# Kernel optimization log

Measured on AMD Instinct MI355X. Metric: run time of the kernel, lower is better.

The kernel has to match this reference:

```python
import jax, jax.numpy as jnp
import numpy as np

TYPE_NUM = 40000
REL_NUM = 10000
N = TYPE_NUM + REL_NUM  # 50000 nodes
E = 800000              # edges (avg degree 16)
EMB, MID, OUT = 256, 256, 128


def setup_inputs() -> dict:
    key = jax.random.key(0)
    k0, k1, k2, k3 = jax.random.split(key, 4)
    # xavier-ish scales
    node_emb = jax.random.normal(k0, (N, EMB), jnp.float32) * (1.0 / np.sqrt(EMB))
    W1 = jax.random.normal(k1, (EMB, MID), jnp.float32) * (1.0 / np.sqrt(EMB))
    W2 = jax.random.normal(k2, (MID, OUT), jnp.float32) * (1.0 / np.sqrt(MID))
    b1 = jnp.zeros((MID,), jnp.float32)
    b2 = jnp.zeros((OUT,), jnp.float32)
    edge_index = jax.random.randint(k3, (2, E), 0, N, jnp.int32)
    return {"node_emb": node_emb, "W1": W1, "b1": b1, "W2": W2, "b2": b2,
            "edge_index": edge_index}


def _gcn_conv(X, W, b, src, dst):
    """torch_geometric GCNConv: x' = D^-1/2 (A+I) D^-1/2 (X W) + b."""
    n = X.shape[0]
    loop = jnp.arange(n, dtype=src.dtype)
    s = jnp.concatenate([src, loop])  # source j
    d = jnp.concatenate([dst, loop])  # target i
    deg = jax.ops.segment_sum(jnp.ones_like(d, dtype=X.dtype), d, num_segments=n)
    dis = jnp.where(deg > 0, jax.lax.rsqrt(deg), 0.0)
    h = X @ W                               # [n, out]
    norm = (dis[s] * dis[d])[:, None]       # [E+n, 1]
    msg = h[s] * norm                       # gather messages
    return jax.ops.segment_sum(msg, d, num_segments=n) + b


def reference(node_emb, W1, b1, W2, b2, edge_index):
    src, dst = edge_index[0], edge_index[1]
    # torch nn.GELU default is exact (erf) gelu
    X = jax.nn.gelu(_gcn_conv(node_emb, W1, b1, src, dst), approximate=False)
    X = jax.nn.gelu(_gcn_conv(X, W2, b2, src, dst), approximate=False)
    return X[:TYPE_NUM], X[TYPE_NUM:]
```

## Files before the change

### kernel.cpp

```cpp
#include <hip/hip_runtime.h>
#include <math.h>

#define EMB 256
#define MID 256
#define OUTF 128
#define KDIM 256
#define LDK 40
#define SLOT 64

using frag_ab = __attribute__((ext_vector_type(8))) short;
using frag_cd = __attribute__((ext_vector_type(4))) float;
typedef float f32x2 __attribute__((ext_vector_type(2)));

__device__ __forceinline__ float gelu_exact(float x) {
    return 0.5f * x * (1.0f + erff(x * 0.70710678118654752f));
}

__device__ __forceinline__ unsigned short f2bf(float f) {
    union { float f; unsigned int i; } v;
    v.f = f;
    unsigned int r = v.i + 0x7fff + ((v.i >> 16) & 1);
    return (unsigned short)(r >> 16);
}

__device__ __forceinline__ f32x2 bfpair(unsigned int u) {
    union { unsigned int i; float f; } a, b;
    a.i = u << 16;
    b.i = u & 0xffff0000u;
    f32x2 r;
    r.x = a.f; r.y = b.f;
    return r;
}


__global__ __launch_bounds__(256) void init_kernel(
    const float* __restrict__ W1, const float* __restrict__ W2,
    unsigned short* __restrict__ W1t, unsigned short* __restrict__ W2t,
    int* __restrict__ cnt, unsigned short* __restrict__ h1pad,
    unsigned short* __restrict__ h2pad, int n, int zb) {
    int b = blockIdx.x;
    int tid = threadIdx.x;
    if (b < zb) {
        int i = b * 256 + tid;
        if (i < n) cnt[i] = 0;
        return;
    }
    b -= zb;
    if (b < 256) {
        int id = b * 256 + tid;
        int k = id >> 8, nn = id & 255;
        W1t[(size_t)nn * EMB + k] = f2bf(W1[(size_t)k * MID + nn]);
        return;
    }
    b -= 256;
    if (b < 128) {
        int id = b * 256 + tid;
        int k = id >> 7, nn = id & 127;
        W2t[(size_t)nn * MID + k] = f2bf(W2[(size_t)k * OUTF + nn]);
        return;
    }
    h1pad[tid] = 0;
    if (tid < OUTF) h2pad[tid] = 0;
}


__global__ void rank_scatter(const int* __restrict__ src, const int* __restrict__ dst,
                             int* __restrict__ cnt, int* __restrict__ slots, int E) {
    int e = blockIdx.x * blockDim.x + threadIdx.x;
    if (e < E) {
        int d = dst[e];
        int r = atomicAdd(&cnt[d], 1);
        if (r < SLOT) slots[(size_t)d * SLOT + r] = src[e];
    }
}


template <bool A_FP32, int NT>
__global__ __launch_bounds__(256, 2) void mfma_gemm(const void* __restrict__ Av,
                                                    const unsigned short* __restrict__ Wt,
                                                    const int* __restrict__ cnt,
                                                    unsigned short* __restrict__ C,
                                                    int M) {
    constexpr int Ntot = NT * 128;
    __shared__ __align__(16) unsigned short As[128 * LDK];
    __shared__ __align__(16) unsigned short Bs[NT * 128 * LDK];

    const int tid = threadIdx.x;
    const int m0 = blockIdx.x * 128;
    const int wave = tid >> 6, lane = tid & 63;
    const int wrow = (wave >> 1) * 64, wcol = (wave & 1) * 64;
    const int q = lane >> 4, r = lane & 15;

    frag_cd acc[NT][4][4] = {};

    const int qb = tid & 3;
    const int nb = tid >> 2;

    for (int ks = 0; ks < KDIM; ks += 32) {
        if (A_FP32) {
            const float* A = (const float*)Av;
            int qa = tid & 7;
            int ra = tid >> 3;
#pragma unroll
            for (int rr = 0; rr < 4; ++rr) {
                int row = ra + rr * 32;
                int grow = m0 + row;
                if (grow >= M) grow = M - 1;
                float4 v = *(const float4*)(A + (size_t)grow * KDIM + ks + qa * 4);
                ushort4 w;
                w.x = f2bf(v.x); w.y = f2bf(v.y); w.z = f2bf(v.z); w.w = f2bf(v.w);
                *(ushort4*)&As[row * LDK + qa * 4] = w;
            }
        } else {
            const unsigned short* A = (const unsigned short*)Av;
#pragma unroll
            for (int rr = 0; rr < 2; ++rr) {
                int row = nb + rr * 64;
                int grow = m0 + row;
                if (grow >= M) grow = M - 1;
                uint4 v = *(const uint4*)(A + (size_t)grow * KDIM + ks + qb * 8);
                *(uint4*)&As[row * LDK + qb * 8] = v;
            }
        }
#pragma unroll
        for (int rr = 0; rr < 2 * NT; ++rr) {
            int n = nb + rr * 64;
            uint4 v = *(const uint4*)(Wt + (size_t)n * KDIM + ks + qb * 8);
            *(uint4*)&Bs[n * LDK + qb * 8] = v;
        }
        __syncthreads();

        frag_ab af[4];
#pragma unroll
        for (int i = 0; i < 4; ++i)
            af[i] = *(const frag_ab*)&As[(wrow + i * 16 + r) * LDK + q * 8];
#pragma unroll
        for (int nt = 0; nt < NT; ++nt) {
            frag_ab bfr[4];
#pragma unroll
            for (int j = 0; j < 4; ++j)
                bfr[j] = *(const frag_ab*)&Bs[(nt * 128 + wcol + j * 16 + r) * LDK + q * 8];
#pragma unroll
            for (int i = 0; i < 4; ++i)
#pragma unroll
                for (int j = 0; j < 4; ++j)
                    acc[nt][i][j] = __builtin_amdgcn_mfma_f32_16x16x32_bf16(
                        af[i], bfr[j], acc[nt][i][j], 0, 0, 0);
        }
        __syncthreads();
    }

#pragma unroll
    for (int i = 0; i < 4; ++i)
#pragma unroll
        for (int g = 0; g < 4; ++g) {
            int row = m0 + wrow + i * 16 + q * 4 + g;
            if (row < M) {
                float sc = rsqrtf((float)(cnt[row] + 1));
#pragma unroll
                for (int nt = 0; nt < NT; ++nt)
#pragma unroll
                    for (int j = 0; j < 4; ++j) {
                        int col = nt * 128 + wcol + j * 16 + r;
                        C[(size_t)row * Ntot + col] = f2bf(acc[nt][i][j][g] * sc);
                    }
            }
        }
}


template <int VEC> struct ldt;
template <> struct ldt<4> { using T = uint2; };
template <> struct ldt<2> { using T = unsigned int; };

template <int F, bool OUT_BF>
__global__ __launch_bounds__(256) void agg_gelu4(const unsigned short* __restrict__ h,
                                                 const int* __restrict__ cnt,
                                                 const int* __restrict__ slots,
                                                 const float* __restrict__ bias,
                                                 void* __restrict__ out, int n) {
    constexpr int VEC = F / 64;
    using LT = typename ldt<VEC>::T;
    int wid = (blockIdx.x * 256 + threadIdx.x) >> 6;
    int lane = threadIdx.x & 63;
    if (wid >= n) return;
    const int c0 = lane * VEC;
    const unsigned short* hb = h + c0;

    int deg = cnt[wid];
    float di = rsqrtf((float)(deg + 1));
    int m = deg < SLOT ? deg : SLOT;

    f32x2 acc[VEC / 2];
    {
        LT s = *(const LT*)(hb + (size_t)wid * F);
        const unsigned int* u = (const unsigned int*)&s;
#pragma unroll
        for (int p = 0; p < VEC / 2; ++p) acc[p] = bfpair(u[p]);
    }

    if (m > 0) {
        int jmine = (lane < m) ? slots[(size_t)wid * SLOT + lane] : n;
        int mp = (m + 7) & ~7;

        LT A[8], B[8];
        auto load8 = [&](LT* buf, int t) {
#pragma unroll
            for (int u = 0; u < 8; ++u) {
                int j = __builtin_amdgcn_readlane(jmine, t + u);
                buf[u] = *(const LT*)(hb + (size_t)j * F);
            }
        };
        auto acc8 = [&](const LT* buf) {
#pragma unroll
            for (int u = 0; u < 8; ++u) {
                const unsigned int* w = (const unsigned int*)&buf[u];
#pragma unroll
                for (int p = 0; p < VEC / 2; ++p) acc[p] += bfpair(w[p]);
            }
        };

        load8(A, 0);
        int t = 8;
        for (;;) {
            if (t >= mp) { acc8(A); break; }
            load8(B, t); acc8(A); t += 8;
            if (t >= mp) { acc8(B); break; }
            load8(A, t); acc8(B); t += 8;
        }
    }

    float res[VEC];
#pragma unroll
    for (int p = 0; p < VEC / 2; ++p) {
        res[2 * p + 0] = gelu_exact(di * acc[p].x + bias[c0 + 2 * p + 0]);
        res[2 * p + 1] = gelu_exact(di * acc[p].y + bias[c0 + 2 * p + 1]);
    }

    if (OUT_BF) {
        unsigned short* ob = (unsigned short*)out + (size_t)wid * F + c0;
        if (VEC == 4) {
            uint2 pk;
            pk.x = (unsigned int)f2bf(res[0]) | ((unsigned int)f2bf(res[1]) << 16);
            pk.y = (unsigned int)f2bf(res[2]) | ((unsigned int)f2bf(res[3]) << 16);
            *(uint2*)ob = pk;
        } else {
            unsigned int pk = (unsigned int)f2bf(res[0]) | ((unsigned int)f2bf(res[1]) << 16);
            *(unsigned int*)ob = pk;
        }
    } else {
        float* ob = (float*)out + (size_t)wid * F + c0;
        if (VEC == 4) {
            float4 rv; rv.x = res[0]; rv.y = res[1]; rv.z = res[2]; rv.w = res[3];
            *(float4*)ob = rv;
        } else {
            float2 rv; rv.x = res[0]; rv.y = res[1];
            *(float2*)ob = rv;
        }
    }
}


extern "C" void kernel_launch(void* const* d_in, const int* in_sizes, int n_in,
                              void* d_out, int out_size, void* d_ws, size_t ws_size,
                              hipStream_t stream) {
    const float* node_emb = (const float*)d_in[0];
    const float* W1 = (const float*)d_in[1];
    const float* b1 = (const float*)d_in[2];
    const float* W2 = (const float*)d_in[3];
    const float* b2 = (const float*)d_in[4];
    const int* edge_index = (const int*)d_in[5];

    const int N = in_sizes[0] / EMB;
    const int E = in_sizes[5] / 2;
    const int* src = edge_index;
    const int* dst = edge_index + E;

    char* ws = (char*)d_ws;
    size_t off = 0;
    auto alloc = [&](size_t bytes) -> void* {
        off = (off + 255) & ~(size_t)255;
        void* p = ws + off;
        off += bytes;
        return p;
    };

    const int nb = (N + 255) / 256;

    int* cnt = (int*)alloc((size_t)N * 4);
    int* slots = (int*)alloc((size_t)N * SLOT * 4);
    unsigned short* W1t = (unsigned short*)alloc((size_t)EMB * MID * 2);
    unsigned short* W2t = (unsigned short*)alloc((size_t)MID * OUTF * 2);
    unsigned short* h1 = (unsigned short*)alloc((size_t)(N + 1) * MID * 2);
    unsigned short* h2 = (unsigned short*)alloc((size_t)(N + 1) * OUTF * 2);
    unsigned short* X1 = (unsigned short*)alloc((size_t)N * MID * 2);

    init_kernel<<<nb + 256 + 128 + 1, 256, 0, stream>>>(
        W1, W2, W1t, W2t, cnt, h1 + (size_t)N * MID, h2 + (size_t)N * OUTF, N, nb);
    rank_scatter<<<(E + 255) / 256, 256, 0, stream>>>(src, dst, cnt, slots, E);
    mfma_gemm<true, 2><<<(N + 127) / 128, 256, 0, stream>>>(node_emb, W1t, cnt, h1, N);
    agg_gelu4<256, true><<<(N + 3) / 4, 256, 0, stream>>>(h1, cnt, slots, b1, X1, N);
    mfma_gemm<false, 1><<<(N + 127) / 128, 256, 0, stream>>>(X1, W2t, cnt, h2, N);
    agg_gelu4<128, false><<<(N + 3) / 4, 256, 0, stream>>>(h2, cnt, slots, b2, d_out, N);
}
```

Before: 259.8 us.

## Slice features into 32-column panels and aggregate per slice for cache locality

Stores h1, h2 and X1 in a column-sliced layout of 32 bf16 features per node, so each aggregation block gathers from one slice that can stay resident in L2/LLC. Aggregation becomes a persistent grid where 8 lane-groups gather neighbors in parallel and reduce with shuffles. Slot indices shrink to 16-bit, which only holds because N is at most 65535, and outputs use nontemporal stores. The cost is redundant cnt and slot reads per slice and more shuffle work.

```diff
diff --git a/kernel.cpp b/kernel.cpp
--- a/kernel.cpp
+++ b/kernel.cpp
@@ -11,6 +11,8 @@
 using frag_ab = __attribute__((ext_vector_type(8))) short;
 using frag_cd = __attribute__((ext_vector_type(4))) float;
 typedef float f32x2 __attribute__((ext_vector_type(2)));
+typedef float f32x4 __attribute__((ext_vector_type(4)));
+typedef unsigned int u32x2 __attribute__((ext_vector_type(2)));
 
 __device__ __forceinline__ float gelu_exact(float x) {
     return 0.5f * x * (1.0f + erff(x * 0.70710678118654752f));
@@ -36,8 +38,8 @@
 __global__ __launch_bounds__(256) void init_kernel(
     const float* __restrict__ W1, const float* __restrict__ W2,
     unsigned short* __restrict__ W1t, unsigned short* __restrict__ W2t,
-    int* __restrict__ cnt, unsigned short* __restrict__ h1pad,
-    unsigned short* __restrict__ h2pad, int n, int zb) {
+    int* __restrict__ cnt, unsigned short* __restrict__ h1,
+    unsigned short* __restrict__ h2, int n, int zb) {
     int b = blockIdx.x;
     int tid = threadIdx.x;
     if (b < zb) {
@@ -59,18 +61,21 @@
         W2t[(size_t)nn * MID + k] = f2bf(W2[(size_t)k * OUTF + nn]);
         return;
     }
-    h1pad[tid] = 0;
-    if (tid < OUTF) h2pad[tid] = 0;
+    size_t Np1 = (size_t)n + 1;
+    int s = tid >> 5, c = tid & 31;
+    h1[((size_t)s * Np1 + n) * 32 + c] = 0;
+    if (tid < 128) h2[((size_t)s * Np1 + n) * 32 + c] = 0;
 }
 
 
 __global__ void rank_scatter(const int* __restrict__ src, const int* __restrict__ dst,
-                             int* __restrict__ cnt, int* __restrict__ slots, int E) {
+                             int* __restrict__ cnt, unsigned short* __restrict__ slots,
+                             int E) {
     int e = blockIdx.x * blockDim.x + threadIdx.x;
     if (e < E) {
         int d = dst[e];
         int r = atomicAdd(&cnt[d], 1);
-        if (r < SLOT) slots[(size_t)d * SLOT + r] = src[e];
+        if (r < SLOT) slots[(size_t)d * SLOT + r] = (unsigned short)src[e];
     }
 }
 
@@ -80,8 +85,7 @@
                                                     const unsigned short* __restrict__ Wt,
                                                     const int* __restrict__ cnt,
                                                     unsigned short* __restrict__ C,
-                                                    int M) {
-    constexpr int Ntot = NT * 128;
+                                                    int M, int Cs) {
     __shared__ __align__(16) unsigned short As[128 * LDK];
     __shared__ __align__(16) unsigned short Bs[NT * 128 * LDK];
 
@@ -118,7 +122,7 @@
                 int row = nb + rr * 64;
                 int grow = m0 + row;
                 if (grow >= M) grow = M - 1;
-                uint4 v = *(const uint4*)(A + (size_t)grow * KDIM + ks + qb * 8);
+                uint4 v = *(const uint4*)(A + ((size_t)(ks >> 5) * M + grow) * 32 + qb * 8);
                 *(uint4*)&As[row * LDK + qb * 8] = v;
             }
         }
@@ -162,100 +166,90 @@
 #pragma unroll
                     for (int j = 0; j < 4; ++j) {
                         int col = nt * 128 + wcol + j * 16 + r;
-                        C[(size_t)row * Ntot + col] = f2bf(acc[nt][i][j][g] * sc);
+                        C[((size_t)(col >> 5) * Cs + row) * 32 + (col & 31)] =
+                            f2bf(acc[nt][i][j][g] * sc);
                     }
             }
         }
 }
 
 
-template <int VEC> struct ldt;
-template <> struct ldt<4> { using T = uint2; };
-template <> struct ldt<2> { using T = unsigned int; };
-
-template <int F, bool OUT_BF>
-__global__ __launch_bounds__(256) void agg_gelu4(const unsigned short* __restrict__ h,
-                                                 const int* __restrict__ cnt,
-                                                 const int* __restrict__ slots,
-                                                 const float* __restrict__ bias,
-                                                 void* __restrict__ out, int n) {
-    constexpr int VEC = F / 64;
-    using LT = typename ldt<VEC>::T;
-    int wid = (blockIdx.x * 256 + threadIdx.x) >> 6;
-    int lane = threadIdx.x & 63;
-    if (wid >= n) return;
-    const int c0 = lane * VEC;
-    const unsigned short* hb = h + c0;
-
-    int deg = cnt[wid];
-    float di = rsqrtf((float)(deg + 1));
-    int m = deg < SLOT ? deg : SLOT;
-
-    f32x2 acc[VEC / 2];
-    {
-        LT s = *(const LT*)(hb + (size_t)wid * F);
-        const unsigned int* u = (const unsigned int*)&s;
-#pragma unroll
-        for (int p = 0; p < VEC / 2; ++p) acc[p] = bfpair(u[p]);
-    }
-
-    if (m > 0) {
-        int jmine = (lane < m) ? slots[(size_t)wid * SLOT + lane] : n;
-        int mp = (m + 7) & ~7;
-
-        LT A[8], B[8];
-        auto load8 = [&](LT* buf, int t) {
-#pragma unroll
-            for (int u = 0; u < 8; ++u) {
-                int j = __builtin_amdgcn_readlane(jmine, t + u);
-                buf[u] = *(const LT*)(hb + (size_t)j * F);
-            }
-        };
-        auto acc8 = [&](const LT* buf) {
-#pragma unroll
-            for (int u = 0; u < 8; ++u) {
-                const unsigned int* w = (const unsigned int*)&buf[u];
-#pragma unroll
-                for (int p = 0; p < VEC / 2; ++p) acc[p] += bfpair(w[p]);
-            }
-        };
-
-        load8(A, 0);
-        int t = 8;
-        for (;;) {
-            if (t >= mp) { acc8(A); break; }
-            load8(B, t); acc8(A); t += 8;
-            if (t >= mp) { acc8(B); break; }
-            load8(A, t); acc8(B); t += 8;
-        }
-    }
-
-    float res[VEC];
-#pragma unroll
-    for (int p = 0; p < VEC / 2; ++p) {
-        res[2 * p + 0] = gelu_exact(di * acc[p].x + bias[c0 + 2 * p + 0]);
-        res[2 * p + 1] = gelu_exact(di * acc[p].y + bias[c0 + 2 * p + 1]);
-    }
-
-    if (OUT_BF) {
-        unsigned short* ob = (unsigned short*)out + (size_t)wid * F + c0;
-        if (VEC == 4) {
-            uint2 pk;
-            pk.x = (unsigned int)f2bf(res[0]) | ((unsigned int)f2bf(res[1]) << 16);
-            pk.y = (unsigned int)f2bf(res[2]) | ((unsigned int)f2bf(res[3]) << 16);
-            *(uint2*)ob = pk;
-        } else {
-            unsigned int pk = (unsigned int)f2bf(res[0]) | ((unsigned int)f2bf(res[1]) << 16);
-            *(unsigned int*)ob = pk;
-        }
-    } else {
-        float* ob = (float*)out + (size_t)wid * F + c0;
-        if (VEC == 4) {
-            float4 rv; rv.x = res[0]; rv.y = res[1]; rv.z = res[2]; rv.w = res[3];
-            *(float4*)ob = rv;
-        } else {
-            float2 rv; rv.x = res[0]; rv.y = res[1];
-            *(float2*)ob = rv;
+template <int NS, bool OUT_BF>
+__global__ __launch_bounds__(256, 8) void agg_slice(
+    const unsigned short* __restrict__ H,
+    const int* __restrict__ cnt,
+    const unsigned short* __restrict__ slots,
+    const float* __restrict__ bias,
+    void* __restrict__ out,
+    int n) {
+    constexpr int XPS = 8 / NS;
+    const int bid = blockIdx.x;
+    const int xg = bid & 7;
+    const int s = xg / XPS;
+    const int w = (bid >> 3) * XPS + (xg % XPS);
+    const int W = (int)(gridDim.x >> 3) * XPS;
+    const int wave = threadIdx.x >> 6, lane = threadIdx.x & 63;
+    const int g = lane >> 3, r = lane & 7;
+    const size_t Np1 = (size_t)n + 1;
+    const unsigned short* Hs = H + (size_t)s * Np1 * 32;
+
+    for (int nd = w * 4 + wave; nd < n; nd += W * 4) {
+        int deg = cnt[nd];
+        float di = rsqrtf((float)(deg + 1));
+        int m = deg < SLOT ? deg : SLOT;
+
+        uint2 sv = *(const uint2*)(Hs + (size_t)nd * 32 + r * 4);
+        f32x2 s01 = bfpair(sv.x), s23 = bfpair(sv.y);
+        float acc[4];
+        acc[0] = g == 0 ? s01.x : 0.f;
+        acc[1] = g == 0 ? s01.y : 0.f;
+        acc[2] = g == 0 ? s23.x : 0.f;
+        acc[3] = g == 0 ? s23.y : 0.f;
+
+        const unsigned short* sl = slots + (size_t)nd * SLOT;
+        int nld = (m + 7) >> 3;
+        uint2 A[8];
+#pragma unroll
+        for (int u = 0; u < 8; ++u) {
+            if (u < nld) {
+                int qn = u * 8 + g;
+                int j = qn < m ? (int)__builtin_nontemporal_load(sl + qn) : n;
+                A[u] = *(const uint2*)(Hs + (size_t)j * 32 + r * 4);
+            }
+        }
+#pragma unroll
+        for (int u = 0; u < 8; ++u) {
+            if (u < nld) {
+                f32x2 p0 = bfpair(A[u].x), p1 = bfpair(A[u].y);
+                acc[0] += p0.x; acc[1] += p0.y; acc[2] += p1.x; acc[3] += p1.y;
+            }
+        }
+
+#pragma unroll
+        for (int k = 0; k < 4; ++k) {
+            acc[k] += __shfl_xor(acc[k], 8);
+            acc[k] += __shfl_xor(acc[k], 16);
+            acc[k] += __shfl_xor(acc[k], 32);
+        }
+
+        if (g == 0) {
+            float4 bv = *(const float4*)(bias + s * 32 + r * 4);
+            float r0 = gelu_exact(di * acc[0] + bv.x);
+            float r1 = gelu_exact(di * acc[1] + bv.y);
+            float r2 = gelu_exact(di * acc[2] + bv.z);
+            float r3 = gelu_exact(di * acc[3] + bv.w);
+            if (OUT_BF) {
+                u32x2 pk;
+                pk.x = (unsigned int)f2bf(r0) | ((unsigned int)f2bf(r1) << 16);
+                pk.y = (unsigned int)f2bf(r2) | ((unsigned int)f2bf(r3) << 16);
+                unsigned short* ob = (unsigned short*)out + ((size_t)s * n + nd) * 32 + r * 4;
+                __builtin_nontemporal_store(pk, (u32x2*)ob);
+            } else {
+                f32x4 rv;
+                rv.x = r0; rv.y = r1; rv.z = r2; rv.w = r3;
+                float* ob = (float*)out + (size_t)nd * (NS * 32) + s * 32 + r * 4;
+                __builtin_nontemporal_store(rv, (f32x4*)ob);
+            }
         }
     }
 }
@@ -288,7 +282,7 @@
     const int nb = (N + 255) / 256;
 
     int* cnt = (int*)alloc((size_t)N * 4);
-    int* slots = (int*)alloc((size_t)N * SLOT * 4);
+    unsigned short* slots = (unsigned short*)alloc((size_t)N * SLOT * 2);
     unsigned short* W1t = (unsigned short*)alloc((size_t)EMB * MID * 2);
     unsigned short* W2t = (unsigned short*)alloc((size_t)MID * OUTF * 2);
     unsigned short* h1 = (unsigned short*)alloc((size_t)(N + 1) * MID * 2);
@@ -296,10 +290,10 @@
     unsigned short* X1 = (unsigned short*)alloc((size_t)N * MID * 2);
 
     init_kernel<<<nb + 256 + 128 + 1, 256, 0, stream>>>(
-        W1, W2, W1t, W2t, cnt, h1 + (size_t)N * MID, h2 + (size_t)N * OUTF, N, nb);
+        W1, W2, W1t, W2t, cnt, h1, h2, N, nb);
     rank_scatter<<<(E + 255) / 256, 256, 0, stream>>>(src, dst, cnt, slots, E);
-    mfma_gemm<true, 2><<<(N + 127) / 128, 256, 0, stream>>>(node_emb, W1t, cnt, h1, N);
-    agg_gelu4<256, true><<<(N + 3) / 4, 256, 0, stream>>>(h1, cnt, slots, b1, X1, N);
-    mfma_gemm<false, 1><<<(N + 127) / 128, 256, 0, stream>>>(X1, W2t, cnt, h2, N);
-    agg_gelu4<128, false><<<(N + 3) / 4, 256, 0, stream>>>(h2, cnt, slots, b2, d_out, N);
-}
+    mfma_gemm<true, 2><<<(N + 127) / 128, 256, 0, stream>>>(node_emb, W1t, cnt, h1, N, N + 1);
+    agg_slice<8, true><<<2048, 256, 0, stream>>>(h1, cnt, slots, b1, X1, N);
+    mfma_gemm<false, 1><<<(N + 127) / 128, 256, 0, stream>>>(X1, W2t, cnt, h2, N, N + 1);
+    agg_slice<4, false><<<2048, 256, 0, stream>>>(h2, cnt, slots, b2, d_out, N);
+}
```

Measured after the change: 393.5 us. 1.51x slower.
